# Performance work log

Measured on AMD Instinct MI355X. Metric: run time of the kernel, lower is better.

## Reference

```python
import jax, jax.numpy as jnp
import numpy as np

B, S, H, V, L = 8, 1024, 1024, 512, 6
NEG_INF = -10000000.0  # matches torch neg_inf constant


def setup_inputs() -> dict:
    key = jax.random.key(0)
    ks = jax.random.split(key, 13)
    s = 0.02
    return {
        "inputs": jax.random.randint(ks[0], (B, S), 0, V),
        "embedding": jax.random.normal(ks[1], (V, H), jnp.float32) * s,
        "Wq": jax.random.normal(ks[2], (L, H, H), jnp.float32) * s,
        "bq": jnp.zeros((L, H), jnp.float32),
        "Wk": jax.random.normal(ks[3], (L, H, H), jnp.float32) * s,
        "bk": jnp.zeros((L, H), jnp.float32),
        "Wv": jax.random.normal(ks[4], (L, H, H), jnp.float32) * s,
        "bv": jnp.zeros((L, H), jnp.float32),
        "Wm": jax.random.normal(ks[5], (L, H, H), jnp.float32) * s,
        "bm": jnp.zeros((L, H), jnp.float32),
        "Wout": jax.random.normal(ks[6], (H, V), jnp.float32) * s,
        "bout": jnp.zeros((V,), jnp.float32),
    }


def reference(inputs, embedding, Wq, bq, Wk, bk, Wv, bv, Wm, bm, Wout, bout):
    Hd = embedding.shape[1]
    seq = inputs.shape[1]
    scale = jax.lax.rsqrt(jnp.asarray(Hd, jnp.float32))
    idx = jnp.arange(seq)
    # mask[key, query]: additive NEG_INF where key > query (strict lower triangle)
    mask = jnp.where(idx[:, None] > idx[None, :], jnp.float32(NEG_INF), jnp.float32(0.0))
    x = embedding[inputs]  # [B, S, H]
    n_layers = Wq.shape[0]
    attns = []
    for l in range(n_layers):
        q = x @ Wq[l] + bq[l]
        k = x @ Wk[l] + bk[l]
        v = x @ Wv[l] + bv[l]
        # [B, key, query], softmax over key axis (dim=1), exactly as original
        logits = jnp.einsum('bkh,bqh->bkq', k, q) * scale + mask
        attn = jax.nn.softmax(logits, axis=1)
        ctx = jnp.einsum('bkq,bkh->bqh', attn, v)  # attn^T @ v
        residual = x + ctx
        x = residual + jax.nn.relu(ctx @ Wm[l] + bm[l])
        attns.append(attn)
    out = x @ Wout + bout  # [B, S, V]
    return out, jnp.stack(attns)  # attns: [L, B, S, S]
```

## Files before the change

### kernel.cpp

```cpp
#include <hip/hip_runtime.h>
#include <stdint.h>

typedef unsigned short u16;
typedef unsigned int u32;
typedef __bf16 bf16x8 __attribute__((ext_vector_type(8)));
typedef float floatx4 __attribute__((ext_vector_type(4)));

#define NEG_INF_F (-10000000.0f)
#define MFMA16 __builtin_amdgcn_mfma_f32_16x16x32_bf16

__device__ __forceinline__ float bf2f(u16 u) {
    union { u32 u; float f; } x; x.u = ((u32)u) << 16; return x.f;
}
__device__ __forceinline__ u16 f2bf(float f) {
    union { float f; u32 u; } x; x.f = f;
    u32 r = x.u + 0x7fffu + ((x.u >> 16) & 1u);
    return (u16)(r >> 16);
}

__device__ __forceinline__ void async_cp16(const void* g, void* l) {
    __builtin_amdgcn_global_load_lds(
        (const __attribute__((address_space(1))) void*)g,
        (__attribute__((address_space(3))) void*)l, 16, 0, 0);
}

enum { EPI_QKV = 0, EPI_LOGITS = 1, EPI_CTX = 2, EPI_MLP = 3, EPI_OUT = 4 };

template <int EPI>
__global__ __launch_bounds__(256) void gemm_bt(
    const u16* __restrict__ A, int lda, long long aBatch,
    const u16* __restrict__ B, int ldb, long long bBatch,
    void* __restrict__ Cv, int ldc, long long cBatch,
    int K,
    const float* __restrict__ bias,
    const u16* __restrict__ ctxb,
    u16* __restrict__ xb,
    float scale, int nx, int ny)
{
    __shared__ __align__(16) u16 sA[128 * 64 + 128];
    __shared__ __align__(16) u16 sB[128 * 64];

    const int tid  = threadIdx.x;
    const int wave = tid >> 6;
    const int lane = tid & 63;

    int bxE, byE, bz;
    if constexpr (EPI == EPI_LOGITS) {
        if (blockIdx.x >= 288) {
            const int t    = blockIdx.x - 288;
            const int b    = t & 7;
            const int tile = t >> 3;
            const int s0 = (tile >> 4) * 64, h0 = (tile & 15) * 64;
            const u16* Vb = ctxb + (long long)b * (1024LL * 3072) + 2 * 1024;
            u16* Ob       = xb   + (long long)b * (1024LL * 1024);
            u32* tl = (u32*)sA;
            const int lr = tid >> 4, lc = tid & 15;
#pragma unroll
            for (int p = 0; p < 4; ++p) {
                const int s = p * 16 + lr;
                uint2 v = *(const uint2*)&Vb[(long long)(s0 + s) * 3072 + h0 + lc * 4];
                tl[s * 65 + lc * 4 + 0] = v.x & 0xffffu;
                tl[s * 65 + lc * 4 + 1] = v.x >> 16;
                tl[s * 65 + lc * 4 + 2] = v.y & 0xffffu;
                tl[s * 65 + lc * 4 + 3] = v.y >> 16;
            }
            __syncthreads();
#pragma unroll
            for (int p = 0; p < 4; ++p) {
                const int h = p * 16 + lr;
                uint2 o;
                o.x = tl[(lc * 4 + 0) * 65 + h] | (tl[(lc * 4 + 1) * 65 + h] << 16);
                o.y = tl[(lc * 4 + 2) * 65 + h] | (tl[(lc * 4 + 3) * 65 + h] << 16);
                *(uint2*)&Ob[(long long)(h0 + h) * 1024 + s0 + lc * 4] = o;
            }
            return;
        }
        bz = blockIdx.x & 7;
        int t = blockIdx.x >> 3;
        int tq = (int)((sqrtf(8.0f * t + 1.0f) - 1.0f) * 0.5f);
        while ((tq + 1) * (tq + 2) / 2 <= t) ++tq;
        while (tq * (tq + 1) / 2 > t) --tq;
        bxE = tq;
        byE = t - tq * (tq + 1) / 2;
    } else if constexpr (EPI == EPI_CTX) {
        bz = blockIdx.x & 7;
        int t = blockIdx.x >> 3;
        bxE = t & 7;
        byE = 7 - (t >> 3);
    } else {
        bz = 0;
        const int k = blockIdx.x & 7, r = blockIdx.x >> 3;
        if (nx >= 8) { const int xp = nx >> 3; bxE = xp * k + (r % xp); byE = r / xp; }
        else         { bxE = k >> 1; byE = (k & 1) * (ny >> 1) + r; }
    }
    int Keff = K;
    if constexpr (EPI == EPI_CTX) Keff = min(K, (byE + 1) * 128);

    const u16* Ab = A + (long long)bz * aBatch + (long long)(byE * 128) * lda;
    const u16* Bb = B + (long long)bz * bBatch + (long long)(bxE * 128) * ldb;

    const int wm = wave >> 1, wn = wave & 1;
    const int quad = lane >> 4;

    const int srowoff = lane >> 3;
    const int gf      = (lane & 7) ^ ((lane >> 3) & 7);

    const int ra = 64 * wm + (lane & 15);
    const int rb = 64 * wn + (lane & 15);
    const int rx7 = lane & 7;

    floatx4 zero = {0.f, 0.f, 0.f, 0.f};
    floatx4 acc[4][4];
#pragma unroll
    for (int i = 0; i < 4; ++i)
#pragma unroll
        for (int j = 0; j < 4; ++j) acc[i][j] = zero;

    for (int k0 = 0; k0 < Keff; k0 += 64) {
#pragma unroll
        for (int i = 0; i < 4; ++i) {
            const int c = wave * 4 + i;
            const int r = c * 8 + srowoff;
            async_cp16(Ab + (long long)r * lda + k0 + gf * 8, &sA[c * 512 + lane * 8]);
            async_cp16(Bb + (long long)r * ldb + k0 + gf * 8, &sB[c * 512 + lane * 8]);
        }
        __syncthreads();

#pragma unroll
        for (int kk = 0; kk < 64; kk += 32) {
            const int gbase = kk >> 3;
            const int ga = ((gbase + quad) ^ rx7) << 3;
            bf16x8 af[4], bf[4];
#pragma unroll
            for (int mi = 0; mi < 4; ++mi)
                af[mi] = *(const bf16x8*)&sA[(ra + 16 * mi) * 64 + ga];
#pragma unroll
            for (int ni = 0; ni < 4; ++ni)
                bf[ni] = *(const bf16x8*)&sB[(rb + 16 * ni) * 64 + ga];
#pragma unroll
            for (int mi = 0; mi < 4; ++mi)
#pragma unroll
                for (int ni = 0; ni < 4; ++ni)
                    acc[mi][ni] = MFMA16(af[mi], bf[ni], acc[mi][ni], 0, 0, 0);
        }
        __syncthreads();
    }

    const int m0 = byE * 128 + 64 * wm + (quad << 2);
    const int n0 = bxE * 128 + 64 * wn + (lane & 15);
#pragma unroll
    for (int mi = 0; mi < 4; ++mi) {
#pragma unroll
        for (int ni = 0; ni < 4; ++ni) {
            const int gn = n0 + ni * 16;
#pragma unroll
            for (int r = 0; r < 4; ++r) {
                const int gm = m0 + mi * 16 + r;
                float v = acc[mi][ni][r];
                if constexpr (EPI == EPI_QKV) {
                    v += bias[gn];
                    ((u16*)Cv)[(long long)gm * ldc + gn] = f2bf(v);
                } else if constexpr (EPI == EPI_LOGITS) {
                    v = v * scale + (gm > gn ? NEG_INF_F : 0.0f);
                    ((float*)Cv)[(long long)bz * cBatch + (long long)gm * ldc + gn] = v;
                } else if constexpr (EPI == EPI_CTX) {
                    ((u16*)Cv)[(long long)bz * cBatch + (long long)gm * ldc + gn] = f2bf(v);
                } else if constexpr (EPI == EPI_MLP) {
                    const long long idx = (long long)gm * ldc + gn;
                    v += bias[gn];
                    v = fmaxf(v, 0.0f);
                    float xv = bf2f(xb[idx]) + bf2f(ctxb[idx]) + v;
                    xb[idx] = f2bf(xv);
                } else {
                    v += bias[gn];
                    ((float*)Cv)[(long long)gm * ldc + gn] = v;
                }
            }
        }
    }
}

template <int L, int H, int V>
__global__ void setup_weights(const float* __restrict__ Wq, const float* __restrict__ Wk,
                              const float* __restrict__ Wv, const float* __restrict__ Wm,
                              const float* __restrict__ Wout,
                              const float* __restrict__ bq, const float* __restrict__ bk,
                              const float* __restrict__ bv,
                              u16* __restrict__ WqkvT, u16* __restrict__ WmT,
                              u16* __restrict__ WoutT, float* __restrict__ bqkv)
{
    const int z = blockIdx.z;
    if (z == 4 * L + 1) {
        int i = ((blockIdx.y * 16 + blockIdx.x) * 256) + threadIdx.y * 64 + threadIdx.x;
        if (i < L * 3 * H) {
            int l = i / (3 * H), j = i % (3 * H);
            float v = (j < H) ? bq[l * H + j]
                    : (j < 2 * H) ? bk[l * H + j - H]
                                  : bv[l * H + j - 2 * H];
            bqkv[i] = v;
        }
        return;
    }

    const float* in;
    u16* outp;
    int inStride, outStride;
    if (z == 4 * L) {
        if (blockIdx.x >= V / 64) return;
        in = Wout; inStride = V;
        outp = WoutT; outStride = H;
    } else {
        const int which = z / L, l = z % L;
        inStride = H; outStride = H;
        if (which == 3) { in = Wm + (long long)l * H * H; outp = WmT + (long long)l * H * H; }
        else {
            in   = (which == 0 ? Wq : which == 1 ? Wk : Wv) + (long long)l * H * H;
            outp = WqkvT + (long long)l * 3 * H * H + (long long)which * H * H;
        }
    }

    __shared__ float tile[64][65];
    const int r0 = blockIdx.y * 64, c0 = blockIdx.x * 64;
    const int x = threadIdx.x, y = threadIdx.y;
#pragma unroll
    for (int j = 0; j < 16; ++j) {
        int r = y + j * 4;
        tile[r][x] = in[(long long)(r0 + r) * inStride + c0 + x];
    }
    __syncthreads();
#pragma unroll
    for (int j = 0; j < 16; ++j) {
        int r = y + j * 4;
        outp[(long long)(c0 + r) * outStride + r0 + x] = f2bf(tile[x][r]);
    }
}

__global__ __launch_bounds__(1024) void attn_post(
    float* __restrict__ attn, long long aStride,
    u16* __restrict__ attnT, long long tStride)
{
    __shared__ float sm[64][16], sl[64][16], sm2[8][16], sl2[8][16];
    __shared__ float sM[16], sInv[16];

    const int b = blockIdx.y;
    float* base = attn + (long long)b * aStride;
    const int x = threadIdx.x, ky = threadIdx.y;
    const int q = blockIdx.x * 16 + x;

    float v[16];
    float m = -3.4e38f, l = 0.f;
#pragma unroll
    for (int j = 0; j < 16; ++j) {
        const int k = ky * 16 + j;
        float vj = NEG_INF_F;
        if (k <= q) vj = base[(long long)k * 1024 + q];
        v[j] = vj;
        float mn = fmaxf(m, vj);
        l = l * __expf(m - mn) + __expf(vj - mn);
        m = mn;
    }
    sm[ky][x] = m;
    sl[ky][x] = l;
    __syncthreads();
    if (ky < 8) {
        float M = -3.4e38f, L = 0.f;
#pragma unroll
        for (int t = 0; t < 8; ++t) {
            float mm = sm[ky + 8 * t][x], ll = sl[ky + 8 * t][x];
            float mn = fmaxf(M, mm);
            L = L * __expf(M - mn) + ll * __expf(mm - mn);
            M = mn;
        }
        sm2[ky][x] = M;
        sl2[ky][x] = L;
    }
    __syncthreads();
    if (ky == 0) {
        float M = -3.4e38f, L = 0.f;
#pragma unroll
        for (int t = 0; t < 8; ++t) {
            float mm = sm2[t][x], ll = sl2[t][x];
            float mn = fmaxf(M, mm);
            L = L * __expf(M - mn) + ll * __expf(mm - mn);
            M = mn;
        }
        sM[x]   = M;
        sInv[x] = 1.0f / L;
    }
    __syncthreads();
    const float M = sM[x], inv = sInv[x];

    u16 pb[16];
#pragma unroll
    for (int j = 0; j < 16; ++j) {
        float p = __expf(v[j] - M) * inv;
        base[(long long)(ky * 16 + j) * 1024 + q] = p;
        pb[j] = f2bf(p);
    }
    u16* trow = attnT + (long long)b * tStride + (long long)q * 1024 + ky * 16;
    ((uint4*)trow)[0] = *(const uint4*)&pb[0];
    ((uint4*)trow)[1] = *(const uint4*)&pb[8];
}

__global__ void embed_kernel(const int* __restrict__ tok, const float* __restrict__ emb,
                             u16* __restrict__ xb)
{
    const int row = blockIdx.x;
    const int t   = tok[row];
    float4 v = ((const float4*)(emb + (long long)t * 1024))[threadIdx.x];
    uint2 p;
    p.x = (u32)f2bf(v.x) | ((u32)f2bf(v.y) << 16);
    p.y = (u32)f2bf(v.z) | ((u32)f2bf(v.w) << 16);
    ((uint2*)(xb + (long long)row * 1024))[threadIdx.x] = p;
}

extern "C" void kernel_launch(void* const* d_in, const int* in_sizes, int n_in,
                              void* d_out, int out_size, void* d_ws, size_t ws_size,
                              hipStream_t stream)
{
    const int*   tok  = (const int*)d_in[0];
    const float* emb  = (const float*)d_in[1];
    const float* Wq   = (const float*)d_in[2];
    const float* bq   = (const float*)d_in[3];
    const float* Wk   = (const float*)d_in[4];
    const float* bk   = (const float*)d_in[5];
    const float* Wv   = (const float*)d_in[6];
    const float* bv   = (const float*)d_in[7];
    const float* Wm   = (const float*)d_in[8];
    const float* bm   = (const float*)d_in[9];
    const float* Wout = (const float*)d_in[10];
    const float* bout = (const float*)d_in[11];
    float* out = (float*)d_out;

    constexpr int B = 8, S = 1024, H = 1024, V = 512, L = 6;
    constexpr long long M = (long long)B * S;

    char* ws = (char*)d_ws;
    u16*   WqkvT = (u16*)ws;   ws += (long long)L * 3 * H * H * 2;
    u16*   WmT   = (u16*)ws;   ws += (long long)L * H * H * 2;
    u16*   WoutT = (u16*)ws;   ws += (long long)V * H * 2;
    float* bqkv  = (float*)ws; ws += (long long)L * 3 * H * 4;
    u16*   xb    = (u16*)ws;   ws += M * H * 2;
    u16*   QKV   = (u16*)ws;   ws += M * 3 * H * 2;
    u16*   attnT = (u16*)ws;   ws += (long long)B * S * S * 2;
    u16*   Vt    = (u16*)ws;   ws += (long long)B * S * S * 2;
    u16*   ctxb  = (u16*)ws;   ws += M * H * 2;

    float* attnOut = out + (long long)B * S * V;

    setup_weights<L, H, V><<<dim3(16, 16, 4 * L + 2), dim3(64, 4), 0, stream>>>(
        Wq, Wk, Wv, Wm, Wout, bq, bk, bv, WqkvT, WmT, WoutT, bqkv);
    embed_kernel<<<M, 256, 0, stream>>>(tok, emb, xb);

    for (int l = 0; l < L; ++l) {
        gemm_bt<EPI_QKV><<<1536, 256, 0, stream>>>(
            xb, H, 0, WqkvT + (long long)l * 3 * H * H, H, 0,
            QKV, 3 * H, 0, H, bqkv + l * 3 * H, nullptr, nullptr, 0.f, 24, 64);

        float* attnL = attnOut + (long long)l * B * S * S;
        gemm_bt<EPI_LOGITS><<<288 + 2048, 256, 0, stream>>>(
            QKV + H, 3 * H, (long long)S * 3 * H,
            QKV, 3 * H, (long long)S * 3 * H,
            attnL, S, (long long)S * S, H,
            nullptr, QKV, Vt, 0.03125f, 0, 0);

        attn_post<<<dim3(64, 8), dim3(16, 64), 0, stream>>>(
            attnL, (long long)S * S, attnT, (long long)S * S);

        gemm_bt<EPI_CTX><<<512, 256, 0, stream>>>(
            attnT, S, (long long)S * S, Vt, S, (long long)S * S,
            ctxb, H, (long long)S * H, S,
            nullptr, nullptr, nullptr, 0.f, 0, 0);

        gemm_bt<EPI_MLP><<<512, 256, 0, stream>>>(
            ctxb, H, 0, WmT + (long long)l * H * H, H, 0,
            nullptr, H, 0, H, bm + l * H, ctxb, xb, 0.f, 8, 64);
    }

    gemm_bt<EPI_OUT><<<256, 256, 0, stream>>>(
        xb, H, 0, WoutT, H, 0, out, V, 0, H,
        bout, nullptr, nullptr, 0.f, 4, 64);
}
```

Before: 1.336 ms.

## Add dedicated 256x256 eight-wave pipelined GEMM kernel for QKV projection

Replaces the generic 128x128 QKV GEMM launch with a new 512-thread kernel that computes 256x256 output tiles, double-buffers A and B tiles in LDS via async global-to-LDS copies, and interleaves loads with MFMA phases under explicit waitcnt/barrier control and s_setprio. Blocks are remapped so groups of eight share operand rows for better L2 reuse. The aim is higher MFMA utilisation and fewer global loads per FLOP in the QKV projection. In exchange the kernel uses a large LDS footprint (128 KB) and heavy register pressure, and its manual vmcnt accounting is fragile.

```diff
diff --git a/kernel.cpp b/kernel.cpp
--- a/kernel.cpp
+++ b/kernel.cpp
@@ -22,6 +22,161 @@
     __builtin_amdgcn_global_load_lds(
         (const __attribute__((address_space(1))) void*)g,
         (__attribute__((address_space(3))) void*)l, 16, 0, 0);
+}
+
+__global__ __launch_bounds__(512, 2) void gemm8p_qkv(
+    const u16* __restrict__ A, int lda,
+    const u16* __restrict__ Bw, int ldb,
+    u16* __restrict__ C, int ldc,
+    int K, const float* __restrict__ bias)
+{
+    __shared__ __align__(16) u16 sA[2][2][128 * 64];
+    __shared__ __align__(16) u16 sB[2][2][128 * 64];
+
+    const int tid  = threadIdx.x;
+    const int wave = tid >> 6;
+    const int lane = tid & 63;
+    const int wm   = wave >> 2;
+    const int wn   = wave & 3;
+    const int quad = lane >> 4;
+    const int l15  = lane & 15;
+    const int l7   = lane & 7;
+
+    const int k8  = blockIdx.x & 7;
+    const int r   = blockIdx.x >> 3;
+    const int bxE = r >> 2;
+    const int byE = k8 * 4 + (r & 3);
+
+    const u16* Ab = A  + (long long)(byE * 256) * lda;
+    const u16* Bb = Bw + (long long)(bxE * 256) * ldb;
+
+    const long long aOff = (long long)(tid >> 3) * lda + (((tid & 7) ^ ((tid >> 3) & 7)) * 8);
+    const long long bOff = (long long)(tid >> 3) * ldb + (((tid & 7) ^ ((tid >> 3) & 7)) * 8);
+    const int dst = tid * 8;
+
+#define STGA8(bf, h, kt) do { \
+    async_cp16(Ab + (long long)((h) * 128) * lda + ((long long)(kt) << 6) + aOff, \
+               &sA[bf][h][dst]); \
+    async_cp16(Ab + (long long)((h) * 128 + 64) * lda + ((long long)(kt) << 6) + aOff, \
+               &sA[bf][h][4096 + dst]); } while (0)
+#define STGB8(bf, h, kt) do { \
+    async_cp16(Bb + (long long)((h) * 128) * ldb + ((long long)(kt) << 6) + bOff, \
+               &sB[bf][h][dst]); \
+    async_cp16(Bb + (long long)((h) * 128 + 64) * ldb + ((long long)(kt) << 6) + bOff, \
+               &sB[bf][h][4096 + dst]); } while (0)
+
+#define AREADS(bf, p) \
+    _Pragma("unroll") for (int h = 0; h < 2; ++h) \
+    _Pragma("unroll") for (int f = 0; f < 2; ++f) \
+        aF[h][f] = *(const bf16x8*)&sA[bf][wm][(((p) * 32 + f * 16 + l15) * 64) \
+                                              + ((((h) << 2) + quad) ^ l7) * 8];
+#define BREADS(bf) \
+    _Pragma("unroll") for (int h = 0; h < 2; ++h) \
+    _Pragma("unroll") for (int ni = 0; ni < 4; ++ni) \
+        bF[h][ni] = *(const bf16x8*)&sB[bf][wn >> 1][(((wn & 1) * 64 + ni * 16 + l15) * 64) \
+                                                    + ((((h) << 2) + quad) ^ l7) * 8];
+#define MFMAS(p) \
+    __builtin_amdgcn_s_barrier(); \
+    asm volatile("s_waitcnt lgkmcnt(0)" ::: "memory"); \
+    __builtin_amdgcn_s_setprio(1); \
+    _Pragma("unroll") for (int h = 0; h < 2; ++h) \
+    _Pragma("unroll") for (int f = 0; f < 2; ++f) \
+    _Pragma("unroll") for (int ni = 0; ni < 4; ++ni) \
+        acc[2 * (p) + f][ni] = MFMA16(aF[h][f], bF[h][ni], acc[2 * (p) + f][ni], 0, 0, 0); \
+    __builtin_amdgcn_s_setprio(0);
+
+    floatx4 acc[8][4];
+#pragma unroll
+    for (int i = 0; i < 8; ++i)
+#pragma unroll
+        for (int j = 0; j < 4; ++j) acc[i][j] = floatx4{0.f, 0.f, 0.f, 0.f};
+
+    bf16x8 bF[2][4];
+
+    const int NT = K >> 6;
+
+    STGA8(0, 0, 0); STGA8(0, 1, 0); STGB8(0, 0, 0); STGB8(0, 1, 0);
+    STGB8(1, 0, 1); STGB8(1, 1, 1);
+    asm volatile("s_waitcnt vmcnt(4)" ::: "memory");
+    __builtin_amdgcn_s_barrier();
+
+    for (int t = 0; t < NT; t += 2) {
+        const bool s2 = (t + 2) < NT;
+
+        {   bf16x8 aF[2][2];
+            AREADS(0, 0); BREADS(0);
+            STGA8(1, 0, t + 1);
+            MFMAS(0);
+            __builtin_amdgcn_s_barrier();
+        }
+        {   bf16x8 aF[2][2];
+            AREADS(0, 1);
+            STGA8(1, 1, t + 1);
+            MFMAS(1);
+            __builtin_amdgcn_s_barrier();
+        }
+        {   bf16x8 aF[2][2];
+            AREADS(0, 2);
+            if (s2) STGB8(0, 0, t + 2);
+            MFMAS(2);
+            __builtin_amdgcn_s_barrier();
+        }
+        {   bf16x8 aF[2][2];
+            AREADS(0, 3);
+            if (s2) STGB8(0, 1, t + 2);
+            MFMAS(3);
+            if (s2) asm volatile("s_waitcnt vmcnt(4)" ::: "memory");
+            else    asm volatile("s_waitcnt vmcnt(0)" ::: "memory");
+            __builtin_amdgcn_s_barrier();
+        }
+        {   bf16x8 aF[2][2];
+            AREADS(1, 0); BREADS(1);
+            if (s2) STGA8(0, 0, t + 2);
+            MFMAS(0);
+            __builtin_amdgcn_s_barrier();
+        }
+        {   bf16x8 aF[2][2];
+            AREADS(1, 1);
+            if (s2) STGA8(0, 1, t + 2);
+            MFMAS(1);
+            __builtin_amdgcn_s_barrier();
+        }
+        {   bf16x8 aF[2][2];
+            AREADS(1, 2);
+            if (s2) STGB8(1, 0, t + 3);
+            MFMAS(2);
+            __builtin_amdgcn_s_barrier();
+        }
+        {   bf16x8 aF[2][2];
+            AREADS(1, 3);
+            if (s2) STGB8(1, 1, t + 3);
+            MFMAS(3);
+            if (s2) asm volatile("s_waitcnt vmcnt(4)" ::: "memory");
+            else    asm volatile("s_waitcnt vmcnt(0)" ::: "memory");
+            __builtin_amdgcn_s_barrier();
+        }
+    }
+#undef STGA8
+#undef STGB8
+#undef AREADS
+#undef BREADS
+#undef MFMAS
+
+    const int m0 = byE * 256 + wm * 128 + (quad << 2);
+    const int n0 = bxE * 256 + wn * 64 + l15;
+#pragma unroll
+    for (int mi = 0; mi < 8; ++mi) {
+#pragma unroll
+        for (int ni = 0; ni < 4; ++ni) {
+            const int gn = n0 + ni * 16;
+            const float bb = bias[gn];
+#pragma unroll
+            for (int rr = 0; rr < 4; ++rr) {
+                const int gm = m0 + mi * 16 + rr;
+                C[(long long)gm * ldc + gn] = f2bf(acc[mi][ni][rr] + bb);
+            }
+        }
+    }
 }
 
 enum { EPI_QKV = 0, EPI_LOGITS = 1, EPI_CTX = 2, EPI_MLP = 3, EPI_OUT = 4 };
@@ -353,9 +508,9 @@
     embed_kernel<<<M, 256, 0, stream>>>(tok, emb, xb);
 
     for (int l = 0; l < L; ++l) {
-        gemm_bt<EPI_QKV><<<1536, 256, 0, stream>>>(
-            xb, H, 0, WqkvT + (long long)l * 3 * H * H, H, 0,
-            QKV, 3 * H, 0, H, bqkv + l * 3 * H, nullptr, nullptr, 0.f, 24, 64);
+        gemm8p_qkv<<<384, 512, 0, stream>>>(
+            xb, H, WqkvT + (long long)l * 3 * H * H, H,
+            QKV, 3 * H, H, bqkv + (long long)l * 3 * H);
 
         float* attnL = attnOut + (long long)l * B * S * S;
         gemm_bt<EPI_LOGITS><<<288 + 2048, 256, 0, stream>>>(
```

Measured after the change: 1.395 ms. 4.4% more time.
